# Kernel optimization log

Measured on AMD Instinct MI355X. Metric: run time of the kernel, lower is better.

## Reference

```python
import jax, jax.numpy as jnp
import numpy as np

CONF = 0.3      # confidence threshold (NMS.conf)
IOU = 0.6       # IoU threshold (NMS.iou)
MAX_WH = 4096.0 # class-offset trick for per-class NMS
K = 2048        # max candidates entering NMS (yolov5-style cap)
MAX_DET = 300   # max detections kept per image (fixed output size)


def setup_inputs() -> dict:
    key = jax.random.key(0)
    kxy, kwh, kobj, kcls = jax.random.split(key, 4)
    B, N, NC = 8, 25200, 80
    # realistic raw predictions: xywh in pixel units for a 640x640 image
    xy = jax.random.uniform(kxy, (B, N, 2), minval=0.0, maxval=640.0)
    wh = jax.random.uniform(kwh, (B, N, 2), minval=2.0, maxval=160.0)
    obj = jax.random.uniform(kobj, (B, N, 1))
    cls = jax.random.uniform(kcls, (B, N, NC))
    x = jnp.concatenate([xy, wh, obj, cls], axis=-1)  # [B, N, 5+NC]
    return {"x": x}


def _xywh2xyxy(b):
    xy, half = b[..., :2], b[..., 2:4] * 0.5
    return jnp.concatenate([xy - half, xy + half], axis=-1)


def _pairwise_iou(boxes):  # boxes: [K, 4] xyxy -> [K, K]
    lt = jnp.maximum(boxes[:, None, :2], boxes[None, :, :2])
    rb = jnp.minimum(boxes[:, None, 2:], boxes[None, :, 2:])
    inter = jnp.clip(rb - lt, 0.0).prod(-1)
    area = (boxes[:, 2] - boxes[:, 0]) * (boxes[:, 3] - boxes[:, 1])
    return inter / (area[:, None] + area[None, :] - inter + 1e-9)


def _nms_single(pred):  # pred: [N, 5+NC]
    obj = pred[:, 4]
    cls_conf = pred[:, 5:] * obj[:, None]          # conf = obj * cls prob
    conf = cls_conf.max(-1)
    cls_id = jnp.argmax(cls_conf, -1)
    valid = (obj > CONF) & (conf > CONF)           # candidate + final threshold
    boxes = _xywh2xyxy(pred[:, :4])
    scores = jnp.where(valid, conf, -1.0)
    top_s, idx = jax.lax.top_k(scores, K)          # cap candidates, sorted desc
    boxes_k = boxes[idx]
    cls_k = cls_id[idx]
    valid_k = top_s > 0.0
    # offset boxes by class so NMS is per-class
    shifted = boxes_k + cls_k[:, None].astype(boxes_k.dtype) * MAX_WH
    iou = _pairwise_iou(shifted)                   # [K, K]
    order = jnp.arange(K)

    def body(keep, i):  # greedy suppression in score order
        active = keep[i] & valid_k[i]
        sup = (iou[i] > IOU) & (order > i)
        keep = jnp.where(active, keep & ~sup, keep)
        return keep, None

    keep, _ = jax.lax.scan(body, jnp.ones((K,), bool), order)
    keep = keep & valid_k
    final_s = jnp.where(keep, top_s, -1.0)
    det_s, det_i = jax.lax.top_k(final_s, MAX_DET)
    dets = jnp.concatenate(
        [boxes_k[det_i], top_s[det_i][:, None],
         cls_k[det_i][:, None].astype(boxes_k.dtype)], axis=-1)  # [MAX_DET, 6]
    return dets, det_s > 0.0


def reference(x):
    # returns (dets [B, MAX_DET, 6] = xyxy,conf,cls ; valid mask [B, MAX_DET])
    return jax.vmap(_nms_single)(x)
```

## Files before the change

kernel.cpp:

```cpp
#include <hip/hip_runtime.h>

#define B 8
#define N 25200
#define ROW 85
#define NC 80
#define K 2048
#define MAXDET 300
#define NBUCKET 4096
#define CAND_CAP 4096
#define NCHUNK 32
#define STILE 64
#define CTR_STRIDE 64

__global__ void __launch_bounds__(256)
nms_score_kernel(const float* __restrict__ x,
                 float* __restrict__ scores,
                 int* __restrict__ cls_id,
                 float4* __restrict__ boxes4,
                 unsigned* __restrict__ done_ctr,
                 unsigned long long* __restrict__ keepbits) {
    int b = blockIdx.y;
    int i0 = blockIdx.x * STILE;
    if (blockIdx.x == 0) {
        if (threadIdx.x == 0) done_ctr[b * CTR_STRIDE] = 0u;
        if (threadIdx.x < NCHUNK) keepbits[b * NCHUNK + threadIdx.x] = 0ULL;
    }
    int rows = N - i0; if (rows > STILE) rows = STILE;
    __shared__ float lx[STILE * ROW];
    {
        const float4* s4 = (const float4*)(x + ((size_t)b * N + i0) * ROW);
        float4* d4 = (float4*)lx;
        int nv = rows * ROW / 4;
        for (int k = threadIdx.x; k < nv; k += 256) d4[k] = s4[k];
    }
    __syncthreads();
    int g = threadIdx.x >> 2;
    int q = threadIdx.x & 3;
    if (g >= rows) return;
    const float* p = lx + g * ROW;
    float obj = p[4];
    float best = -1e30f;
    int bc = 127;
    if (obj > 0.3f) {
        #pragma unroll
        for (int k = 0; k < 20; ++k) {
            int c = q + 4 * k;
            float v = __fmul_rn(p[5 + c], obj);
            if (v > best) { best = v; bc = c; }
        }
    }
    #pragma unroll
    for (int m = 1; m < 4; m <<= 1) {
        float ov = __shfl_xor(best, m, 64);
        int   oc = __shfl_xor(bc, m, 64);
        if (ov > best || (ov == best && oc < bc)) { best = ov; bc = oc; }
    }
    if (q == 0) {
        int i = i0 + g;
        float score = (obj > 0.3f && best > 0.3f) ? best : -1.0f;
        scores[b * N + i] = score;
        cls_id[b * N + i] = (bc == 127) ? 0 : bc;
        float cx = p[0], cy = p[1], w = p[2], h = p[3];
        float hx = __fmul_rn(w, 0.5f);
        float hy = __fmul_rn(h, 0.5f);
        boxes4[b * N + i] = make_float4(__fsub_rn(cx, hx), __fsub_rn(cy, hy),
                                        __fadd_rn(cx, hx), __fadd_rn(cy, hy));
    }
}

__global__ void __launch_bounds__(1024, 1)
nms_tail_kernel(const float* __restrict__ scores,
                const float4* __restrict__ boxes4,
                const int* __restrict__ cls_id,
                unsigned long long* __restrict__ keepbits,
                unsigned* __restrict__ done_ctr,
                float* __restrict__ out) {
    __shared__ union {
        struct {
            unsigned loff[NBUCKET];
            unsigned lcnt16[NBUCKET / 2];
            unsigned long long lk[CAND_CAP];
        } s;
        struct {
            unsigned long long keys[K];
            unsigned long long lcm[NC * NCHUNK];
            unsigned long long kept[NCHUNK];
            unsigned kcpref[NCHUNK];
            int total;
            int oflag;
        } c;
    } U;
    __shared__ unsigned wsum[16];

    int bid = blockIdx.x;
    int t = threadIdx.x;
    int ln = t & 63, wv = t >> 6;
    unsigned long long below = (ln == 0) ? 0ULL : (~0ULL >> (64 - ln));

    int b = bid / 5;
    int grp = bid % 5;
    int c = grp * 16 + wv;
    constexpr int NITER = (N + 1023) / 1024;

    {
        uint4 z = {0u, 0u, 0u, 0u};
        uint4* d1 = (uint4*)U.s.loff;
        for (int k = t; k < (NBUCKET + NBUCKET / 2) / 4; k += 1024) d1[k] = z;
    }
    for (int k = t; k < CAND_CAP; k += 1024) U.s.lk[k] = 0ULL;
    __syncthreads();

    float sreg[NITER];
    #pragma unroll
    for (int r = 0; r < NITER; ++r) {
        int i = t + r * 1024;
        float s = (i < N) ? scores[b * N + i] : -1.0f;
        sreg[r] = s;
        if (s > 0.0f) {
            int q = (int)(__fmul_rn(s, 4096.0f));
            if (q > NBUCKET - 1) q = NBUCKET - 1;
            atomicAdd(&U.s.loff[q], 1u);
        }
    }
    __syncthreads();

    {
        unsigned v[4];
        unsigned A4 = (unsigned)(NBUCKET / 4 - 1 - t);
        {
            uint4 u0 = ((uint4*)U.s.loff)[A4];
            v[0] = u0.w; v[1] = u0.z; v[2] = u0.y; v[3] = u0.x;
        }
        unsigned S = v[0] + v[1] + v[2] + v[3];
        unsigned pref = S;
        #pragma unroll
        for (int o = 1; o < 64; o <<= 1) { unsigned u = __shfl_up(pref, o, 64); if (ln >= o) pref += u; }
        if (ln == 63) wsum[wv] = pref;
        __syncthreads();
        unsigned wbase = 0;
        for (int w = 0; w < wv; ++w) wbase += wsum[w];
        unsigned running = wbase + pref - S;
        unsigned o[4];
        #pragma unroll
        for (int k = 0; k < 4; ++k) { o[3 - k] = running; running += v[k]; }
        ((uint4*)U.s.loff)[A4] = make_uint4(o[0], o[1], o[2], o[3]);
    }
    __syncthreads();

    #pragma unroll
    for (int r = 0; r < NITER; ++r) {
        float s = sreg[r];
        if (s > 0.0f) {
            int i = t + r * 1024;
            int q = (int)(__fmul_rn(s, 4096.0f));
            if (q > NBUCKET - 1) q = NBUCKET - 1;
            unsigned start = U.s.loff[q];
            if (start < CAND_CAP) {
                unsigned sh = (q & 1) * 16;
                unsigned old = atomicAdd(&U.s.lcnt16[q >> 1], 1u << sh);
                unsigned rank = (old >> sh) & 0xFFFFu;
                unsigned pos = start + rank;
                if (pos < CAND_CAP) {
                    unsigned long long key =
                        ((unsigned long long)__float_as_uint(s) << 32) | (unsigned)(~i);
                    U.s.lk[pos] = key;
                }
            }
        }
    }
    __syncthreads();

    for (int q = t; q < NBUCKET; q += 1024) {
        unsigned start = U.s.loff[q];
        if (start < CAND_CAP) {
            unsigned cc = (U.s.lcnt16[q >> 1] >> ((q & 1) * 16)) & 0xFFFFu;
            unsigned m = cc;
            if (m > CAND_CAP - start) m = CAND_CAP - start;
            if (m >= 2) {
                for (unsigned a = start + 1; a < start + m; ++a) {
                    unsigned long long kv = U.s.lk[a];
                    unsigned p2 = a;
                    while (p2 > start && U.s.lk[p2 - 1] < kv) { U.s.lk[p2] = U.s.lk[p2 - 1]; --p2; }
                    U.s.lk[p2] = kv;
                }
            }
        }
    }
    __syncthreads();

    for (int r = t; r < K; r += 1024) U.c.keys[r] = U.s.lk[r];
    __syncthreads();
    for (int k = t; k < NC * NCHUNK; k += 1024) U.c.lcm[k] = 0ULL;
    if (t == 0) U.c.oflag = 0;
    __syncthreads();

    for (int r = t; r < K; r += 1024) {
        unsigned long long key = U.c.keys[r];
        if (key != 0ULL) {
            int idx = (int)(~(unsigned)key);
            int cc = cls_id[b * N + idx];
            atomicOr(&U.c.lcm[cc * NCHUNK + (r >> 6)], 1ULL << (r & 63));
        }
    }
    __syncthreads();

    int n = 0, r = -1, ch_i = -1, myk = -1;
    unsigned long long mych = 0ULL;
    for (int ch = 0; ch < NCHUNK; ++ch) {
        unsigned long long m = U.c.lcm[c * NCHUNK + ch];
        int cnt = __popcll(m);
        if (myk < 0 && ln < n + cnt) { mych = m; myk = ln - n; ch_i = ch; }
        n += cnt;
    }
    if (myk >= 0) {
        unsigned long long mm = mych;
        for (int z = 0; z < myk; ++z) mm &= mm - 1;
        r = ch_i * 64 + (int)__builtin_ctzll(mm);
    }

    float shf = __fmul_rn((float)c, 4096.0f);

    if (n > 0 && n <= 64) {
        float x1 = 0.f, y1 = 0.f, x2 = 0.f, y2 = 0.f, ar = 0.f;
        if (ln < n) {
            unsigned long long key = U.c.keys[r];
            int idx = (int)(~(unsigned)key);
            float4 bb = boxes4[(size_t)b * N + idx];
            x1 = __fadd_rn(bb.x, shf); y1 = __fadd_rn(bb.y, shf);
            x2 = __fadd_rn(bb.z, shf); y2 = __fadd_rn(bb.w, shf);
            ar = __fmul_rn(__fsub_rn(x2, x1), __fsub_rn(y2, y1));
        }
        unsigned long long keepw = (n == 64) ? ~0ULL : ((1ULL << n) - 1ULL);
        for (int i = 0; i < n; ++i) {
            if (!((keepw >> i) & 1ULL)) continue;
            float bx1 = __shfl(x1, i, 64), by1 = __shfl(y1, i, 64);
            float bx2 = __shfl(x2, i, 64), by2 = __shfl(y2, i, 64);
            float ba  = __shfl(ar, i, 64);
            bool cond = false;
            if (ln > i && ln < n) {
                float lx = fmaxf(bx1, x1), ly = fmaxf(by1, y1);
                float rx = fminf(bx2, x2), ry = fminf(by2, y2);
                float w = fmaxf(__fsub_rn(rx, lx), 0.0f);
                float h = fmaxf(__fsub_rn(ry, ly), 0.0f);
                float inter = __fmul_rn(w, h);
                float denom = __fadd_rn(__fsub_rn(__fadd_rn(ba, ar), inter), 1e-9f);
                cond = __fdiv_rn(inter, denom) > 0.6f;
            }
            keepw &= ~__ballot(cond);
        }
        if (ln < n && ((keepw >> ln) & 1ULL))
            atomicOr(&keepbits[b * NCHUNK + (r >> 6)], 1ULL << (r & 63));
    } else if (n > 64) {
        unsigned long long membw = (ln < NCHUNK) ? U.c.lcm[c * NCHUNK + ln] : 0ULL;
        unsigned long long keepw2 = membw;
        for (int i = 0; i < K; ++i) {
            int ch = i >> 6;
            unsigned long long mw = __shfl(membw, ch, 64);
            unsigned long long kw = __shfl(keepw2, ch, 64);
            unsigned long long bi = 1ULL << (i & 63);
            if (!(mw & kw & bi)) continue;
            unsigned long long keyi = U.c.keys[i];
            int idxi = (int)(~(unsigned)keyi);
            float4 bi4 = boxes4[(size_t)b * N + idxi];
            float bx1 = __fadd_rn(bi4.x, shf), by1 = __fadd_rn(bi4.y, shf);
            float bx2 = __fadd_rn(bi4.z, shf), by2 = __fadd_rn(bi4.w, shf);
            float ba = __fmul_rn(__fsub_rn(bx2, bx1), __fsub_rn(by2, by1));
            for (int c2 = ch; c2 < NCHUNK; ++c2) {
                int j = c2 * 64 + ln;
                unsigned long long mw2 = __shfl(membw, c2, 64);
                bool cond = false;
                if (j > i && ((mw2 >> ln) & 1ULL)) {
                    unsigned long long keyj = U.c.keys[j];
                    int idxj = (int)(~(unsigned)keyj);
                    float4 bj4 = boxes4[(size_t)b * N + idxj];
                    float x1 = __fadd_rn(bj4.x, shf), y1 = __fadd_rn(bj4.y, shf);
                    float x2 = __fadd_rn(bj4.z, shf), y2 = __fadd_rn(bj4.w, shf);
                    float arj = __fmul_rn(__fsub_rn(x2, x1), __fsub_rn(y2, y1));
                    float lx = fmaxf(bx1, x1), ly = fmaxf(by1, y1);
                    float rx = fminf(bx2, x2), ry = fminf(by2, y2);
                    float w = fmaxf(__fsub_rn(rx, lx), 0.0f);
                    float h = fmaxf(__fsub_rn(ry, ly), 0.0f);
                    float inter = __fmul_rn(w, h);
                    float denom = __fadd_rn(__fsub_rn(__fadd_rn(ba, arj), inter), 1e-9f);
                    cond = __fdiv_rn(inter, denom) > 0.6f;
                }
                unsigned long long sup = __ballot(cond);
                if (ln == c2) keepw2 &= ~sup;
            }
        }
        if (ln < NCHUNK && (keepw2 & membw))
            atomicOr(&keepbits[b * NCHUNK + ln], keepw2 & membw);
    }

    __threadfence();
    unsigned old = 0;
    if (ln == 0) old = atomicAdd(&done_ctr[b * CTR_STRIDE], 1u);
    old = (unsigned)__shfl((int)old, 0, 64);
    if (old == NC - 1) {
        __threadfence();
        unsigned long long kwv = 0ULL;
        if (ln < NCHUNK) kwv = atomicOr(&keepbits[b * NCHUNK + ln], 0ULL);
        unsigned pc = (unsigned)__popcll(kwv);
        unsigned incl = pc;
        #pragma unroll
        for (int o = 1; o < 32; o <<= 1) { unsigned u = __shfl_up(incl, o, 64); if (ln >= o) incl += u; }
        if (ln < NCHUNK) {
            U.c.kept[ln] = kwv;
            U.c.kcpref[ln] = incl - pc;
        }
        if (ln == 31) U.c.total = (int)incl;
        if (ln == 0)  U.c.oflag = 1;
    }
    __syncthreads();

    if (U.c.oflag) {
        int total = U.c.total;
        float* dets  = out + (size_t)b * MAXDET * 6;
        float* flags = out + (size_t)B * MAXDET * 6 + (size_t)b * MAXDET;
        #pragma unroll
        for (int h = 0; h < 2; ++h) {
            int ch = wv * 2 + h;
            int i = ch * 64 + ln;
            unsigned long long m = U.c.kept[ch];
            bool k = ((m >> ln) & 1ULL) != 0ULL;
            int kp = (int)U.c.kcpref[ch];
            int np = ch * 64 - kp;
            int slot = k ? (kp + (int)__popcll(m & below))
                         : (total + np + (int)__popcll((~m) & below));
            if (slot < MAXDET) {
                unsigned long long key = U.c.keys[i];
                float s, ox1, oy1, ox2, oy2; int oc;
                if (key == 0ULL) {
                    s = -1.0f; ox1 = oy1 = ox2 = oy2 = 0.0f; oc = 0;
                } else {
                    s = __uint_as_float((unsigned)(key >> 32));
                    int idx = (int)(~(unsigned)key);
                    float4 bb = boxes4[(size_t)b * N + idx];
                    ox1 = bb.x; oy1 = bb.y; ox2 = bb.z; oy2 = bb.w;
                    oc = cls_id[b * N + idx];
                }
                dets[slot * 6 + 0] = ox1;
                dets[slot * 6 + 1] = oy1;
                dets[slot * 6 + 2] = ox2;
                dets[slot * 6 + 3] = oy2;
                dets[slot * 6 + 4] = s;
                dets[slot * 6 + 5] = (float)oc;
                flags[slot] = k ? 1.0f : 0.0f;
            }
        }
    }
}

extern "C" void kernel_launch(void* const* d_in, const int* in_sizes, int n_in,
                              void* d_out, int out_size, void* d_ws, size_t ws_size,
                              hipStream_t stream) {
    const float* x = (const float*)d_in[0];
    float* out = (float*)d_out;

    char* ws = (char*)d_ws;
    size_t off = 0;
    auto alloc = [&](size_t bytes) -> void* {
        void* p = ws + off;
        off += bytes;
        off = (off + 255) & ~(size_t)255;
        return p;
    };

    float*    scores = (float*)    alloc((size_t)B * N * 4);
    int*      cls_id = (int*)      alloc((size_t)B * N * 4);
    float4*   boxes4 = (float4*)   alloc((size_t)B * N * 16);
    unsigned long long* keepbits = (unsigned long long*) alloc((size_t)B * NCHUNK * 8);
    unsigned* done_ctr = (unsigned*) alloc((size_t)B * CTR_STRIDE * 4);
    (void)ws_size;

    nms_score_kernel<<<dim3((N + STILE - 1) / STILE, B), 256, 0, stream>>>(
        x, scores, cls_id, boxes4, done_ctr, keepbits);
    nms_tail_kernel<<<5 * B, 1024, 0, stream>>>(
        scores, boxes4, cls_id, keepbits, done_ctr, out);
}
```

Baseline: 136.3 us.

## Use one tail block per image and loop over class rounds locally

The tail kernel now runs one block per image instead of five. Each block processes all 80 classes in five rounds of 16 waves and accumulates keep bits in shared memory. This removes the global keepbits and done-counter atomics, the threadfences, and the last-block-finishes election, along with the redundant candidate bucketing and sort that each of the five blocks per image used to repeat. The cost is five times fewer tail blocks (only 8), with each block doing the class-wise NMS work serially, which lowers parallelism on a large GPU.

```diff
diff --git a/kernel.cpp b/kernel.cpp
--- a/kernel.cpp
+++ b/kernel.cpp
@@ -10,21 +10,14 @@
 #define CAND_CAP 4096
 #define NCHUNK 32
 #define STILE 64
-#define CTR_STRIDE 64
 
 __global__ void __launch_bounds__(256)
 nms_score_kernel(const float* __restrict__ x,
                  float* __restrict__ scores,
                  int* __restrict__ cls_id,
-                 float4* __restrict__ boxes4,
-                 unsigned* __restrict__ done_ctr,
-                 unsigned long long* __restrict__ keepbits) {
+                 float4* __restrict__ boxes4) {
     int b = blockIdx.y;
     int i0 = blockIdx.x * STILE;
-    if (blockIdx.x == 0) {
-        if (threadIdx.x == 0) done_ctr[b * CTR_STRIDE] = 0u;
-        if (threadIdx.x < NCHUNK) keepbits[b * NCHUNK + threadIdx.x] = 0ULL;
-    }
     int rows = N - i0; if (rows > STILE) rows = STILE;
     __shared__ float lx[STILE * ROW];
     {
@@ -72,8 +65,6 @@
 nms_tail_kernel(const float* __restrict__ scores,
                 const float4* __restrict__ boxes4,
                 const int* __restrict__ cls_id,
-                unsigned long long* __restrict__ keepbits,
-                unsigned* __restrict__ done_ctr,
                 float* __restrict__ out) {
     __shared__ union {
         struct {
@@ -84,22 +75,18 @@
         struct {
             unsigned long long keys[K];
             unsigned long long lcm[NC * NCHUNK];
+            unsigned long long lkeep[NCHUNK];
             unsigned long long kept[NCHUNK];
             unsigned kcpref[NCHUNK];
             int total;
-            int oflag;
         } c;
     } U;
     __shared__ unsigned wsum[16];
 
-    int bid = blockIdx.x;
+    int b = blockIdx.x;
     int t = threadIdx.x;
     int ln = t & 63, wv = t >> 6;
     unsigned long long below = (ln == 0) ? 0ULL : (~0ULL >> (64 - ln));
-
-    int b = bid / 5;
-    int grp = bid % 5;
-    int c = grp * 16 + wv;
     constexpr int NITER = (N + 1023) / 1024;
 
     {
@@ -191,7 +178,7 @@
     for (int r = t; r < K; r += 1024) U.c.keys[r] = U.s.lk[r];
     __syncthreads();
     for (int k = t; k < NC * NCHUNK; k += 1024) U.c.lcm[k] = 0ULL;
-    if (t == 0) U.c.oflag = 0;
+    if (t < NCHUNK) U.c.lkeep[t] = 0ULL;
     __syncthreads();
 
     for (int r = t; r < K; r += 1024) {
@@ -204,102 +191,102 @@
     }
     __syncthreads();
 
-    int n = 0, r = -1, ch_i = -1, myk = -1;
-    unsigned long long mych = 0ULL;
-    for (int ch = 0; ch < NCHUNK; ++ch) {
-        unsigned long long m = U.c.lcm[c * NCHUNK + ch];
-        int cnt = __popcll(m);
-        if (myk < 0 && ln < n + cnt) { mych = m; myk = ln - n; ch_i = ch; }
-        n += cnt;
-    }
-    if (myk >= 0) {
-        unsigned long long mm = mych;
-        for (int z = 0; z < myk; ++z) mm &= mm - 1;
-        r = ch_i * 64 + (int)__builtin_ctzll(mm);
-    }
-
-    float shf = __fmul_rn((float)c, 4096.0f);
-
-    if (n > 0 && n <= 64) {
-        float x1 = 0.f, y1 = 0.f, x2 = 0.f, y2 = 0.f, ar = 0.f;
-        if (ln < n) {
-            unsigned long long key = U.c.keys[r];
-            int idx = (int)(~(unsigned)key);
-            float4 bb = boxes4[(size_t)b * N + idx];
-            x1 = __fadd_rn(bb.x, shf); y1 = __fadd_rn(bb.y, shf);
-            x2 = __fadd_rn(bb.z, shf); y2 = __fadd_rn(bb.w, shf);
-            ar = __fmul_rn(__fsub_rn(x2, x1), __fsub_rn(y2, y1));
-        }
-        unsigned long long keepw = (n == 64) ? ~0ULL : ((1ULL << n) - 1ULL);
-        for (int i = 0; i < n; ++i) {
-            if (!((keepw >> i) & 1ULL)) continue;
-            float bx1 = __shfl(x1, i, 64), by1 = __shfl(y1, i, 64);
-            float bx2 = __shfl(x2, i, 64), by2 = __shfl(y2, i, 64);
-            float ba  = __shfl(ar, i, 64);
-            bool cond = false;
-            if (ln > i && ln < n) {
-                float lx = fmaxf(bx1, x1), ly = fmaxf(by1, y1);
-                float rx = fminf(bx2, x2), ry = fminf(by2, y2);
-                float w = fmaxf(__fsub_rn(rx, lx), 0.0f);
-                float h = fmaxf(__fsub_rn(ry, ly), 0.0f);
-                float inter = __fmul_rn(w, h);
-                float denom = __fadd_rn(__fsub_rn(__fadd_rn(ba, ar), inter), 1e-9f);
-                cond = __fdiv_rn(inter, denom) > 0.6f;
-            }
-            keepw &= ~__ballot(cond);
-        }
-        if (ln < n && ((keepw >> ln) & 1ULL))
-            atomicOr(&keepbits[b * NCHUNK + (r >> 6)], 1ULL << (r & 63));
-    } else if (n > 64) {
-        unsigned long long membw = (ln < NCHUNK) ? U.c.lcm[c * NCHUNK + ln] : 0ULL;
-        unsigned long long keepw2 = membw;
-        for (int i = 0; i < K; ++i) {
-            int ch = i >> 6;
-            unsigned long long mw = __shfl(membw, ch, 64);
-            unsigned long long kw = __shfl(keepw2, ch, 64);
-            unsigned long long bi = 1ULL << (i & 63);
-            if (!(mw & kw & bi)) continue;
-            unsigned long long keyi = U.c.keys[i];
-            int idxi = (int)(~(unsigned)keyi);
-            float4 bi4 = boxes4[(size_t)b * N + idxi];
-            float bx1 = __fadd_rn(bi4.x, shf), by1 = __fadd_rn(bi4.y, shf);
-            float bx2 = __fadd_rn(bi4.z, shf), by2 = __fadd_rn(bi4.w, shf);
-            float ba = __fmul_rn(__fsub_rn(bx2, bx1), __fsub_rn(by2, by1));
-            for (int c2 = ch; c2 < NCHUNK; ++c2) {
-                int j = c2 * 64 + ln;
-                unsigned long long mw2 = __shfl(membw, c2, 64);
+    for (int round = 0; round < 5; ++round) {
+        int c = round * 16 + wv;
+
+        int n = 0, r = -1, ch_i = -1, myk = -1;
+        unsigned long long mych = 0ULL;
+        for (int ch = 0; ch < NCHUNK; ++ch) {
+            unsigned long long m = U.c.lcm[c * NCHUNK + ch];
+            int cnt = __popcll(m);
+            if (myk < 0 && ln < n + cnt) { mych = m; myk = ln - n; ch_i = ch; }
+            n += cnt;
+        }
+        if (myk >= 0) {
+            unsigned long long mm = mych;
+            for (int z = 0; z < myk; ++z) mm &= mm - 1;
+            r = ch_i * 64 + (int)__builtin_ctzll(mm);
+        }
+
+        float shf = __fmul_rn((float)c, 4096.0f);
+
+        if (n > 0 && n <= 64) {
+            float x1 = 0.f, y1 = 0.f, x2 = 0.f, y2 = 0.f, ar = 0.f;
+            if (ln < n) {
+                unsigned long long key = U.c.keys[r];
+                int idx = (int)(~(unsigned)key);
+                float4 bb = boxes4[(size_t)b * N + idx];
+                x1 = __fadd_rn(bb.x, shf); y1 = __fadd_rn(bb.y, shf);
+                x2 = __fadd_rn(bb.z, shf); y2 = __fadd_rn(bb.w, shf);
+                ar = __fmul_rn(__fsub_rn(x2, x1), __fsub_rn(y2, y1));
+            }
+            unsigned long long keepw = (n == 64) ? ~0ULL : ((1ULL << n) - 1ULL);
+            for (int i = 0; i < n; ++i) {
+                if (!((keepw >> i) & 1ULL)) continue;
+                float bx1 = __shfl(x1, i, 64), by1 = __shfl(y1, i, 64);
+                float bx2 = __shfl(x2, i, 64), by2 = __shfl(y2, i, 64);
+                float ba  = __shfl(ar, i, 64);
                 bool cond = false;
-                if (j > i && ((mw2 >> ln) & 1ULL)) {
-                    unsigned long long keyj = U.c.keys[j];
-                    int idxj = (int)(~(unsigned)keyj);
-                    float4 bj4 = boxes4[(size_t)b * N + idxj];
-                    float x1 = __fadd_rn(bj4.x, shf), y1 = __fadd_rn(bj4.y, shf);
-                    float x2 = __fadd_rn(bj4.z, shf), y2 = __fadd_rn(bj4.w, shf);
-                    float arj = __fmul_rn(__fsub_rn(x2, x1), __fsub_rn(y2, y1));
+                if (ln > i && ln < n) {
                     float lx = fmaxf(bx1, x1), ly = fmaxf(by1, y1);
                     float rx = fminf(bx2, x2), ry = fminf(by2, y2);
                     float w = fmaxf(__fsub_rn(rx, lx), 0.0f);
                     float h = fmaxf(__fsub_rn(ry, ly), 0.0f);
                     float inter = __fmul_rn(w, h);
-                    float denom = __fadd_rn(__fsub_rn(__fadd_rn(ba, arj), inter), 1e-9f);
+                    float denom = __fadd_rn(__fsub_rn(__fadd_rn(ba, ar), inter), 1e-9f);
                     cond = __fdiv_rn(inter, denom) > 0.6f;
                 }
-                unsigned long long sup = __ballot(cond);
-                if (ln == c2) keepw2 &= ~sup;
-            }
-        }
-        if (ln < NCHUNK && (keepw2 & membw))
-            atomicOr(&keepbits[b * NCHUNK + ln], keepw2 & membw);
-    }
-
-    __threadfence();
-    unsigned old = 0;
-    if (ln == 0) old = atomicAdd(&done_ctr[b * CTR_STRIDE], 1u);
-    old = (unsigned)__shfl((int)old, 0, 64);
-    if (old == NC - 1) {
-        __threadfence();
-        unsigned long long kwv = 0ULL;
-        if (ln < NCHUNK) kwv = atomicOr(&keepbits[b * NCHUNK + ln], 0ULL);
+                keepw &= ~__ballot(cond);
+            }
+            if (ln < n && ((keepw >> ln) & 1ULL))
+                atomicOr(&U.c.lkeep[r >> 6], 1ULL << (r & 63));
+        } else if (n > 64) {
+            unsigned long long membw = (ln < NCHUNK) ? U.c.lcm[c * NCHUNK + ln] : 0ULL;
+            unsigned long long keepw2 = membw;
+            for (int i = 0; i < K; ++i) {
+                int ch = i >> 6;
+                unsigned long long mw = __shfl(membw, ch, 64);
+                unsigned long long kw = __shfl(keepw2, ch, 64);
+                unsigned long long bi = 1ULL << (i & 63);
+                if (!(mw & kw & bi)) continue;
+                unsigned long long keyi = U.c.keys[i];
+                int idxi = (int)(~(unsigned)keyi);
+                float4 bi4 = boxes4[(size_t)b * N + idxi];
+                float bx1 = __fadd_rn(bi4.x, shf), by1 = __fadd_rn(bi4.y, shf);
+                float bx2 = __fadd_rn(bi4.z, shf), by2 = __fadd_rn(bi4.w, shf);
+                float ba = __fmul_rn(__fsub_rn(bx2, bx1), __fsub_rn(by2, by1));
+                for (int c2 = ch; c2 < NCHUNK; ++c2) {
+                    int j = c2 * 64 + ln;
+                    unsigned long long mw2 = __shfl(membw, c2, 64);
+                    bool cond = false;
+                    if (j > i && ((mw2 >> ln) & 1ULL)) {
+                        unsigned long long keyj = U.c.keys[j];
+                        int idxj = (int)(~(unsigned)keyj);
+                        float4 bj4 = boxes4[(size_t)b * N + idxj];
+                        float x1 = __fadd_rn(bj4.x, shf), y1 = __fadd_rn(bj4.y, shf);
+                        float x2 = __fadd_rn(bj4.z, shf), y2 = __fadd_rn(bj4.w, shf);
+                        float arj = __fmul_rn(__fsub_rn(x2, x1), __fsub_rn(y2, y1));
+                        float lx = fmaxf(bx1, x1), ly = fmaxf(by1, y1);
+                        float rx = fminf(bx2, x2), ry = fminf(by2, y2);
+                        float w = fmaxf(__fsub_rn(rx, lx), 0.0f);
+                        float h = fmaxf(__fsub_rn(ry, ly), 0.0f);
+                        float inter = __fmul_rn(w, h);
+                        float denom = __fadd_rn(__fsub_rn(__fadd_rn(ba, arj), inter), 1e-9f);
+                        cond = __fdiv_rn(inter, denom) > 0.6f;
+                    }
+                    unsigned long long sup = __ballot(cond);
+                    if (ln == c2) keepw2 &= ~sup;
+                }
+            }
+            unsigned long long kb = keepw2 & membw;
+            if (ln < NCHUNK && kb)
+                atomicOr(&U.c.lkeep[ln], kb);
+        }
+    }
+    __syncthreads();
+
+    if (wv == 0) {
+        unsigned long long kwv = (ln < NCHUNK) ? U.c.lkeep[ln] : 0ULL;
         unsigned pc = (unsigned)__popcll(kwv);
         unsigned incl = pc;
         #pragma unroll
@@ -309,11 +296,10 @@
             U.c.kcpref[ln] = incl - pc;
         }
         if (ln == 31) U.c.total = (int)incl;
-        if (ln == 0)  U.c.oflag = 1;
-    }
-    __syncthreads();
-
-    if (U.c.oflag) {
+    }
+    __syncthreads();
+
+    {
         int total = U.c.total;
         float* dets  = out + (size_t)b * MAXDET * 6;
         float* flags = out + (size_t)B * MAXDET * 6 + (size_t)b * MAXDET;
@@ -366,15 +352,12 @@
         return p;
     };
 
-    float*    scores = (float*)    alloc((size_t)B * N * 4);
-    int*      cls_id = (int*)      alloc((size_t)B * N * 4);
-    float4*   boxes4 = (float4*)   alloc((size_t)B * N * 16);
-    unsigned long long* keepbits = (unsigned long long*) alloc((size_t)B * NCHUNK * 8);
-    unsigned* done_ctr = (unsigned*) alloc((size_t)B * CTR_STRIDE * 4);
+    float*  scores = (float*)  alloc((size_t)B * N * 4);
+    int*    cls_id = (int*)    alloc((size_t)B * N * 4);
+    float4* boxes4 = (float4*) alloc((size_t)B * N * 16);
     (void)ws_size;
 
     nms_score_kernel<<<dim3((N + STILE - 1) / STILE, B), 256, 0, stream>>>(
-        x, scores, cls_id, boxes4, done_ctr, keepbits);
-    nms_tail_kernel<<<5 * B, 1024, 0, stream>>>(
-        scores, boxes4, cls_id, keepbits, done_ctr, out);
+        x, scores, cls_id, boxes4);
+    nms_tail_kernel<<<B, 1024, 0, stream>>>(scores, boxes4, cls_id, out);
 }
```

Result: slower. 175.7 us (+29.0%).
